# Performance work log

Hardware: AMD Instinct MI355X
Metric: run time of the kernel (lower is better)

The kernel has to match this reference:

```python
import jax, jax.numpy as jnp
import numpy as np

NUM_HEADS = 3
WIN = 7            # window_size (square)
PAD = WIN // 2     # conv / v padding


def setup_inputs() -> dict:
    key = jax.random.key(0)
    ks = jax.random.split(key, 8)
    B, C, H, W = 8, 96, 56, 56
    hd = C // NUM_HEADS  # 32
    x = jax.random.normal(ks[0], (B, C, H, W), jnp.float32)
    # qkv 1x1 conv: weight (3C, C), bias (3C,)
    w_qkv = jax.random.normal(ks[1], (3 * C, C), jnp.float32) * (C ** -0.5)
    b_qkv = jax.random.normal(ks[2], (3 * C,), jnp.float32) * 0.01
    fan_in = 2 * hd * WIN * WIN
    w_dm = jax.random.normal(ks[3], (WIN * WIN, 2 * hd, WIN, WIN), jnp.float32) * (fan_in ** -0.5)
    b_dm = jax.random.normal(ks[4], (WIN * WIN,), jnp.float32) * 0.01
    bias_table = jax.random.normal(ks[5], (WIN * WIN, NUM_HEADS), jnp.float32) * 0.02
    # proj 1x1 conv
    w_proj = jax.random.normal(ks[6], (C, C), jnp.float32) * (C ** -0.5)
    b_proj = jax.random.normal(ks[7], (C,), jnp.float32) * 0.01
    return dict(x=x, w_qkv=w_qkv, b_qkv=b_qkv, w_dm=w_dm, b_dm=b_dm,
                bias_table=bias_table, w_proj=w_proj, b_proj=b_proj)


def reference(x, w_qkv, b_qkv, w_dm, b_dm, bias_table, w_proj, b_proj):
    B, C, H, W = x.shape
    nh = NUM_HEADS
    hd = C // nh
    scale = hd ** -0.5

    # qkv 1x1 conv -> (B, 3, nh, hd, H, W)
    qkv = jnp.einsum('oc,bchw->bohw', w_qkv, x) + b_qkv[None, :, None, None]
    qkv = qkv.reshape(B, 3, nh, hd, H, W)
    q, k, v = qkv[:, 0], qkv[:, 1], qkv[:, 2]

    qk = jnp.concatenate([(q * scale).reshape(B * nh, hd, H, W),
                          k.reshape(B * nh, hd, H, W)], axis=1)
    attn = jax.lax.conv_general_dilated(
        qk, w_dm, window_strides=(1, 1), padding=[(PAD, PAD), (PAD, PAD)],
        dimension_numbers=('NCHW', 'OIHW', 'NCHW')) + b_dm[None, :, None, None]
    attn = attn.reshape(B, nh, WIN * WIN, H, W)

    # relative position bias, broadcast over spatial dims
    attn = attn + bias_table.T.reshape(1, nh, WIN * WIN, 1, 1)
    attn = jax.nn.softmax(attn, axis=2)

    # gather sliding windows of v from a zero-padded tensor
    v_pad = jnp.pad(v, ((0, 0), (0, 0), (0, 0), (PAD, PAD), (PAD, PAD)))
    vw = jnp.stack([v_pad[..., i // WIN:i // WIN + H, i % WIN:i % WIN + W]
                    for i in range(WIN * WIN)], axis=3)

    # weighted sum over window dim, merge heads back to channels
    out = jnp.sum(vw * attn[:, :, None], axis=3).reshape(B, C, H, W)

    # output 1x1 projection (dropout p=0 -> identity)
    out = jnp.einsum('oc,bchw->bohw', w_proj, out) + b_proj[None, :, None, None]
    return out
```

## Files before the change

kernel.cpp:

```cpp
#include <hip/hip_runtime.h>
#include <hip/hip_bf16.h>
#include <stdint.h>

#define BATCH 8
#define CCH 96
#define NH 3
#define HD 32
#define HGT 56
#define WID 56
#define HW 3136
#define WIN 7
#define KK 49
#define PADR 3
#define NIMG 24
#define C2 64

typedef const float* fp32p;
typedef __attribute__((ext_vector_type(8))) short bf16x8;
typedef __attribute__((ext_vector_type(16))) float f32x16;
typedef __attribute__((ext_vector_type(2))) float f32x2;
typedef unsigned short ushort_t;

__device__ __forceinline__ float bf2f_bits(unsigned u){ return __uint_as_float(u << 16); }
__device__ __forceinline__ ushort_t f2bf_bits(float f){
  __hip_bfloat16 hb = __float2bfloat16(f);
  return *(ushort_t*)&hb;
}

__global__ __launch_bounds__(256) void prep_kernel(fp32p w_dm, fp32p b_dm,
    fp32p bias_table, fp32p w_qkv, fp32p w_proj,
    __hip_bfloat16* __restrict__ w3, float* __restrict__ bias3,
    ushort_t* __restrict__ wq3, ushort_t* __restrict__ wp3){
  int t = blockIdx.x * 256 + threadIdx.x;
  if (t < 200704){
    int j   = t & 7;
    int l   = (t >> 3) & 63;
    int mt  = (t >> 9) & 1;
    int cb  = (t >> 10) & 1;
    int pt  = t >> 11;
    int pass = pt / KK, tap = pt % KK;
    int o  = mt*32 + (l & 31);
    int ch = pass*32 + cb*16 + (l >> 5)*8 + j;
    float v = 0.f;
    if (o < KK) v = w_dm[((size_t)(o*C2 + ch))*KK + tap];
    w3[t] = __float2bfloat16(v);
  } else if (t < 200896){
    int t2 = t - 200704;
    int h = t2 >> 6;
    int o = t2 & 63;
    bias3[t2] = (o < KK) ? (b_dm[o] + bias_table[o*NH + h]) : -1e30f;
  } else if (t < 200896 + 27648){
    int i = t - 200896;
    int j = i & 7, l = (i >> 3) & 63;
    int rest = i >> 9;
    int mt = rest % 9, k = rest / 9;
    int o = mt*32 + (l & 31);
    int c = k*16 + (l >> 5)*8 + j;
    wq3[i] = f2bf_bits(w_qkv[o*CCH + c]);
  } else if (t < 200896 + 27648 + 9216){
    int i = t - 200896 - 27648;
    int j = i & 7, l = (i >> 3) & 63;
    int rest = i >> 9;
    int mt = rest % 3, k = rest / 3;
    int o = mt*32 + (l & 31);
    int c = k*16 + (l >> 5)*8 + j;
    wp3[i] = f2bf_bits(w_proj[o*CCH + c]);
  }
}

__global__ __launch_bounds__(64) void qkv_kernel(fp32p x,
    const ushort_t* __restrict__ wq3, fp32p b_qkv,
    ushort_t* __restrict__ qplane, ushort_t* __restrict__ kplane,
    ushort_t* __restrict__ v2){
  __shared__ float lds[32*97];
  int wid = blockIdx.x;
  int g  = wid / 784;
  int pt = wid % 784;
  int l = threadIdx.x & 63, col = l & 31, hi = l >> 5;
  int b = pt / 98;
  int pp0 = (pt % 98) * 32;
  int pp = pp0 + col;

  #pragma unroll
  for (int it = 0; it < 48; ++it){
    int s = (int)threadIdx.x + it*64;
    int c = s >> 5, pxi = s & 31;
    lds[pxi*97 + c] = x[((size_t)b*CCH + c)*HW + pp0 + pxi];
  }
  __syncthreads();

  bf16x8 B[6];
  #pragma unroll
  for (int k = 0; k < 6; ++k){
    unsigned u[4];
    #pragma unroll
    for (int q = 0; q < 4; ++q){
      float f0 = lds[col*97 + k*16 + hi*8 + 2*q];
      float f1 = lds[col*97 + k*16 + hi*8 + 2*q + 1];
      u[q] = (unsigned)f2bf_bits(f0) | ((unsigned)f2bf_bits(f1) << 16);
    }
    unsigned* bp = (unsigned*)&B[k];
    bp[0] = u[0]; bp[1] = u[1]; bp[2] = u[2]; bp[3] = u[3];
  }

  f32x16 acc[3];
  #pragma unroll
  for (int m = 0; m < 3; ++m)
    #pragma unroll
    for (int r = 0; r < 16; ++r) acc[m][r] = 0.f;

  #pragma unroll
  for (int k = 0; k < 6; ++k){
    #pragma unroll
    for (int m = 0; m < 3; ++m){
      bf16x8 A = *(const bf16x8*)((const char*)wq3 + ((size_t)((k*9 + g*3 + m)*64 + l))*16);
      acc[m] = __builtin_amdgcn_mfma_f32_32x32x16_bf16(A, B[k], acc[m], 0, 0, 0);
    }
  }
  const float scale = 0.17677669529663687f;
  ushort_t* plane = (g == 0) ? qplane : (g == 1 ? kplane : v2);
  #pragma unroll
  for (int m = 0; m < 3; ++m){
    ushort_t* dst = plane + ((size_t)((b*NH + m)*HW + pp))*32;
    #pragma unroll
    for (int q = 0; q < 4; ++q){
      int base = 8*q + 4*hi;
      float v0 = acc[m][q*4+0] + b_qkv[g*96 + m*32 + base + 0];
      float v1 = acc[m][q*4+1] + b_qkv[g*96 + m*32 + base + 1];
      float v2f = acc[m][q*4+2] + b_qkv[g*96 + m*32 + base + 2];
      float v3 = acc[m][q*4+3] + b_qkv[g*96 + m*32 + base + 3];
      if (g == 0){ v0 *= scale; v1 *= scale; v2f *= scale; v3 *= scale; }
      uint2 pk;
      pk.x = (unsigned)f2bf_bits(v0) | ((unsigned)f2bf_bits(v1) << 16);
      pk.y = (unsigned)f2bf_bits(v2f) | ((unsigned)f2bf_bits(v3) << 16);
      *(uint2*)(&dst[base]) = pk;
    }
  }
}

#define MFMA4K(Ab, Bb) \
  { _Pragma("unroll") for (int nt = 0; nt < 2; ++nt){ \
      acc[0][nt] = __builtin_amdgcn_mfma_f32_32x32x16_bf16(Ab[0], Bb[nt], acc[0][nt], 0, 0, 0); \
      acc[1][nt] = __builtin_amdgcn_mfma_f32_32x32x16_bf16(Ab[1], Bb[nt], acc[1][nt], 0, 0, 0); \
    } }

#define LOADAK(tt, Ab) \
  { const char* An_ = Abase + (size_t)(tt)*4096; \
    Ab[0] = *(const bf16x8*)(An_); \
    Ab[1] = *(const bf16x8*)(An_ + 1024); }

#define LOADBK(tt, Bb) \
  { int ky_ = (tt) / 7, kx_ = (tt) - ky_*7; \
    _Pragma("unroll") for (int nt = 0; nt < 2; ++nt){ \
      int xp_ = nt*32 + col + kx_; if (xp_ > 61) xp_ = 61; \
      int base_ = ((row + ky_)*64 + xp_)*64; \
      int sx_ = (xp_ & 3) ^ ((xp_ >> 2) & 3); \
      Bb[nt] = *(const bf16x8*)(&smem[base_ + ((((cbw << 1) | hi) ^ sx_) << 4)]); } }

#define XWRITE(A0v, A1v) \
  { _Pragma("unroll") for (int q = 0; q < 4; ++q){ \
      float4 v4; \
      v4.x=A0v[4*q+0]; v4.y=A0v[4*q+1]; v4.z=A0v[4*q+2]; v4.w=A0v[4*q+3]; \
      *(float4*)((char*)xch + slot_o*256 + (((2*q+hi) ^ xsw)<<4)) = v4; \
      v4.x=A1v[4*q+0]; v4.y=A1v[4*q+1]; v4.z=A1v[4*q+2]; v4.w=A1v[4*q+3]; \
      *(float4*)((char*)xch + slot_o*256 + (((8+2*q+hi) ^ xsw)<<4)) = v4; } }

#define XREAD(A0v, A1v) \
  { _Pragma("unroll") for (int q = 0; q < 4; ++q){ \
      float4 v4 = *(const float4*)((char*)xch + slot_s*256 + (((2*q+hi) ^ xsw)<<4)); \
      A0v[4*q+0]+=v4.x; A0v[4*q+1]+=v4.y; A0v[4*q+2]+=v4.z; A0v[4*q+3]+=v4.w; \
      v4 = *(const float4*)((char*)xch + slot_s*256 + (((8+2*q+hi) ^ xsw)<<4)); \
      A1v[4*q+0]+=v4.x; A1v[4*q+1]+=v4.y; A1v[4*q+2]+=v4.z; A1v[4*q+3]+=v4.w; } }

__global__ __launch_bounds__(256, 3) void attn_kernel(
    const ushort_t* __restrict__ qplane, const ushort_t* __restrict__ kplane,
    const __hip_bfloat16* __restrict__ w3, const float* __restrict__ bias3,
    const ushort_t* __restrict__ v2, ushort_t* __restrict__ tmp2){
  __shared__ char smem[50176];

  int d = blockIdx.x;
  int bid = (d & 7)*84 + (d >> 3);
  int n  = bid / 28;
  int y0 = (bid % 28) * 2;
  int b = n / NH, head = n % NH;
  int tid = threadIdx.x;
  int l = tid & 63, w = tid >> 6, hi = l >> 5, col = l & 31;
  int row = w >> 1;
  int cbw = w & 1;

  f32x16 acc[2][2];
  #pragma unroll
  for (int r = 0; r < 16; ++r){
    int rowv = (r & 3) + 8*(r >> 2) + 4*hi;
    float b0 = (cbw == 0) ? bias3[head*64 + rowv] : 0.f;
    float b1 = (cbw == 0) ? bias3[head*64 + 32 + rowv] : 0.f;
    #pragma unroll
    for (int nt = 0; nt < 2; ++nt){ acc[0][nt][r] = b0; acc[1][nt][r] = b1; }
  }

  for (int pass = 0; pass < 2; ++pass){
    if (pass) __syncthreads();
    const char* src = (const char*)(pass ? kplane : qplane) + (size_t)n * HW * 64;
    #pragma unroll
    for (int it = 0; it < 8; ++it){
      int s = tid + it*256;
      int c   = s & 3;
      int xp  = (s >> 2) & 63;
      int rw  = s >> 8;
      int gy = y0 - 3 + rw;
      int gx = xp - 3;
      uint4 val = {0,0,0,0};
      if ((unsigned)gy < HGT && (unsigned)gx < WID)
        val = *(const uint4*)(src + (size_t)(gy*WID + gx)*64 + c*16);
      int sw = (c ^ (xp & 3) ^ ((xp >> 2) & 3)) << 4;
      *(uint4*)(&smem[(rw*64 + xp)*64 + sw]) = val;
    }
    __syncthreads();

    const char* Abase = (const char*)w3 + (size_t)pass*KK*4096 + cbw*2048 + l*16;
    bf16x8 A0[2], A1[2], B0[2], B1[2];
    LOADAK(0, A0); LOADBK(0, B0);
    LOADAK(1, A1); LOADBK(1, B1);
    for (int t = 0; t < 48; t += 2){
      MFMA4K(A0, B0);
      LOADAK(t+2, A0); LOADBK(t+2, B0);
      MFMA4K(A1, B1);
      int t3 = (t+3 < KK) ? (t+3) : 48;
      LOADAK(t3, A1); LOADBK(t3, B1);
    }
    MFMA4K(A0, B0);
  }

  __syncthreads();
  float* xch = (float*)smem;
  int xsw = col & 15;
  {
    int slot_o = row*64 + (1-cbw)*32 + col;
    if (cbw == 0){ XWRITE(acc[0][1], acc[1][1]); }
    else         { XWRITE(acc[0][0], acc[1][0]); }
  }
  __syncthreads();
  f32x16 a0, a1;
  {
    int slot_s = row*64 + cbw*32 + col;
    if (cbw == 0){ XREAD(acc[0][0], acc[1][0]); a0 = acc[0][0]; a1 = acc[1][0]; }
    else         { XREAD(acc[0][1], acc[1][1]); a0 = acc[0][1]; a1 = acc[1][1]; }
  }

  const char* vb = (const char*)v2 + (size_t)n * HW * 64;
  uint4 vreg[8];
  #pragma unroll
  for (int it = 0; it < 8; ++it){
    int s = tid + it*256;
    int xp  = s & 63;
    int c   = (s >> 6) & 3;
    int rw  = s >> 8;
    int gy = y0 - 3 + rw;
    int gx = xp - 3;
    uint4 val = {0,0,0,0};
    if ((unsigned)gy < HGT && (unsigned)gx < WID)
      val = *(const uint4*)(vb + (size_t)(gy*WID + gx)*64 + c*16);
    vreg[it] = val;
  }

  ushort_t* Pp = (ushort_t*)&smem[32768];
  {
    float m = -1e30f;
    #pragma unroll
    for (int r = 0; r < 16; ++r){ m = fmaxf(m, a0[r]); m = fmaxf(m, a1[r]); }
    m = fmaxf(m, __shfl_xor(m, 32));
    float s = 0.f;
    #pragma unroll
    for (int r = 0; r < 16; ++r){
      a0[r] = __expf(a0[r] - m); s += a0[r];
      a1[r] = __expf(a1[r] - m); s += a1[r];
    }
    s += __shfl_xor(s, 32);
    float inv = 1.f / s;
    int pixslot = row*64 + cbw*32 + col;
    ushort_t* Pr = Pp + pixslot*68;
    #pragma unroll
    for (int q = 0; q < 4; ++q){
      int base = 8*q + 4*hi;
      uint2 pk0;
      pk0.x = (unsigned)f2bf_bits(a0[q*4+0]*inv) | ((unsigned)f2bf_bits(a0[q*4+1]*inv) << 16);
      pk0.y = (unsigned)f2bf_bits(a0[q*4+2]*inv) | ((unsigned)f2bf_bits(a0[q*4+3]*inv) << 16);
      *(uint2*)(&Pr[base]) = pk0;
      uint2 pk1;
      pk1.x = (unsigned)f2bf_bits(a1[q*4+0]*inv) | ((unsigned)f2bf_bits(a1[q*4+1]*inv) << 16);
      pk1.y = (unsigned)f2bf_bits(a1[q*4+2]*inv) | ((unsigned)f2bf_bits(a1[q*4+3]*inv) << 16);
      *(uint2*)(&Pr[32 + base]) = pk1;
    }
  }
  __syncthreads();

  #pragma unroll
  for (int it = 0; it < 8; ++it){
    int s = tid + it*256;
    int xp  = s & 63;
    int c   = (s >> 6) & 3;
    int rw  = s >> 8;
    *(uint4*)(&smem[((c*8 + rw)*64 + xp)*16]) = vreg[it];
  }
  __syncthreads();

  int ch2 = tid >> 7;
  int slot = tid & 127;
  int pr = slot >> 6, pxx = slot & 63;
  if (pxx < WID){
    f32x2 out2[8];
    #pragma unroll
    for (int i = 0; i < 8; ++i){ out2[i].x = 0.f; out2[i].y = 0.f; }
    #pragma unroll
    for (int ky = 0; ky < WIN; ++ky){
      #pragma unroll
      for (int kx = 0; kx < WIN; ++kx){
        float pw = bf2f_bits(Pp[slot*68 + ky*7 + kx]);
        f32x2 pw2; pw2.x = pw; pw2.y = pw;
        int vrow = pr + ky, xp = pxx + kx;
        #pragma unroll
        for (int ci = 0; ci < 2; ++ci){
          int cc = ch2*2 + ci;
          uint4 vv = *(const uint4*)(&smem[((cc*8 + vrow)*64 + xp)*16]);
          unsigned ua[4] = {vv.x, vv.y, vv.z, vv.w};
          #pragma unroll
          for (int q = 0; q < 4; ++q){
            f32x2 v2f;
            v2f.x = __uint_as_float(ua[q] << 16);
            v2f.y = __uint_as_float(ua[q] & 0xffff0000u);
            out2[ci*4 + q] += pw2 * v2f;
          }
        }
      }
    }
    int pp = (y0 + pr)*WID + pxx;
    ushort_t* dst = tmp2 + ((size_t)(b*HW + pp))*96 + head*32 + ch2*16;
    #pragma unroll
    for (int j2 = 0; j2 < 2; ++j2){
      unsigned u[4];
      #pragma unroll
      for (int q = 0; q < 4; ++q){
        u[q] = (unsigned)f2bf_bits(out2[j2*4 + q].x) | ((unsigned)f2bf_bits(out2[j2*4 + q].y) << 16);
      }
      uint4 w4; w4.x=u[0]; w4.y=u[1]; w4.z=u[2]; w4.w=u[3];
      *(uint4*)(&dst[j2*8]) = w4;
    }
  }
}

__global__ __launch_bounds__(64) void proj_kernel(const ushort_t* __restrict__ tmp2,
    const ushort_t* __restrict__ wp3, fp32p b_proj, float* __restrict__ outp){
  int pt = blockIdx.x;
  int l = threadIdx.x & 63, col = l & 31, hi = l >> 5;
  int px = pt*32 + col;
  int b = px / HW, pp = px % HW;

  bf16x8 B[6];
  const char* bb = (const char*)tmp2 + (size_t)px*192 + hi*16;
  #pragma unroll
  for (int k = 0; k < 6; ++k) B[k] = *(const bf16x8*)(bb + k*32);

  f32x16 acc[3];
  #pragma unroll
  for (int m = 0; m < 3; ++m)
    #pragma unroll
    for (int r = 0; r < 16; ++r) acc[m][r] = 0.f;

  #pragma unroll
  for (int k = 0; k < 6; ++k){
    #pragma unroll
    for (int m = 0; m < 3; ++m){
      bf16x8 A = *(const bf16x8*)((const char*)wp3 + ((size_t)((k*3 + m)*64 + l))*16);
      acc[m] = __builtin_amdgcn_mfma_f32_32x32x16_bf16(A, B[k], acc[m], 0, 0, 0);
    }
  }
  #pragma unroll
  for (int m = 0; m < 3; ++m){
    #pragma unroll
    for (int r = 0; r < 16; ++r){
      int o = m*32 + (r & 3) + 8*(r >> 2) + 4*hi;
      outp[((size_t)(b*CCH + o))*HW + pp] = acc[m][r] + b_proj[o];
    }
  }
}

extern "C" void kernel_launch(void* const* d_in, const int* in_sizes, int n_in,
                              void* d_out, int out_size, void* d_ws, size_t ws_size,
                              hipStream_t stream){
  fp32p x          = (fp32p)d_in[0];
  fp32p w_qkv      = (fp32p)d_in[1];
  fp32p b_qkv      = (fp32p)d_in[2];
  fp32p w_dm       = (fp32p)d_in[3];
  fp32p b_dm       = (fp32p)d_in[4];
  fp32p bias_table = (fp32p)d_in[5];
  fp32p w_proj     = (fp32p)d_in[6];
  fp32p b_proj     = (fp32p)d_in[7];

  char* ws = (char*)d_ws;
  const size_t PLANE_BYTES = (size_t)NIMG * HW * 32 * 2;
  const size_t TMP2_BYTES  = (size_t)BATCH * HW * 96 * 2;
  const size_t W3_BYTES    = 200704ull * 2;
  size_t off = 0;
  ushort_t* qplane = (ushort_t*)(ws + off); off += PLANE_BYTES;
  ushort_t* kplane = (ushort_t*)(ws + off); off += PLANE_BYTES;
  ushort_t* v2     = (ushort_t*)(ws + off); off += PLANE_BYTES;
  ushort_t* tmp2   = (ushort_t*)(ws + off); off += TMP2_BYTES;
  __hip_bfloat16* w3 = (__hip_bfloat16*)(ws + off); off += W3_BYTES;
  float* bias3     = (float*)(ws + off);    off += 192*4;
  ushort_t* wq3    = (ushort_t*)(ws + off); off += 27648*2;
  ushort_t* wp3    = (ushort_t*)(ws + off); off += 9216*2;

  hipLaunchKernelGGL(prep_kernel, dim3(929), dim3(256), 0, stream,
                     w_dm, b_dm, bias_table, w_qkv, w_proj, w3, bias3, wq3, wp3);
  hipLaunchKernelGGL(qkv_kernel, dim3(2352), dim3(64), 0, stream,
                     x, wq3, b_qkv, qplane, kplane, v2);
  hipLaunchKernelGGL(attn_kernel, dim3(672), dim3(256), 0, stream,
                     qplane, kplane, w3, bias3, v2, tmp2);
  hipLaunchKernelGGL(proj_kernel, dim3(784), dim3(64), 0, stream,
                     tmp2, wp3, b_proj, (float*)d_out);
}
```

Before: 71.25 us.

## Fuse weight prep into qkv kernel and share x tile across q/k/v

Merges the weight-preparation kernel and the qkv projection kernel into one launch: the first 784 blocks compute qkv with three wavefronts (one per q/k/v group) sharing a single LDS tile of x, and the remaining blocks repack w_dm, bias and w_proj. The qkv weights are now read directly from fp32 and converted to bf16 in registers, so the separate wq3 staging buffer is dropped. The aims are to remove one kernel launch and to avoid loading each x tile three times. In exchange, every qkv block redoes the weight conversion and issues uncoalesced fp32 weight loads.

```diff
diff --git a/kernel.cpp b/kernel.cpp
--- a/kernel.cpp
+++ b/kernel.cpp
@@ -27,63 +27,56 @@
   return *(ushort_t*)&hb;
 }
 
-__global__ __launch_bounds__(256) void prep_kernel(fp32p w_dm, fp32p b_dm,
-    fp32p bias_table, fp32p w_qkv, fp32p w_proj,
+__global__ __launch_bounds__(192) void qkv_prep_kernel(fp32p x, fp32p w_qkv,
+    fp32p b_qkv, fp32p w_dm, fp32p b_dm, fp32p bias_table, fp32p w_proj,
+    ushort_t* __restrict__ qplane, ushort_t* __restrict__ kplane,
+    ushort_t* __restrict__ v2,
     __hip_bfloat16* __restrict__ w3, float* __restrict__ bias3,
-    ushort_t* __restrict__ wq3, ushort_t* __restrict__ wp3){
-  int t = blockIdx.x * 256 + threadIdx.x;
-  if (t < 200704){
-    int j   = t & 7;
-    int l   = (t >> 3) & 63;
-    int mt  = (t >> 9) & 1;
-    int cb  = (t >> 10) & 1;
-    int pt  = t >> 11;
-    int pass = pt / KK, tap = pt % KK;
-    int o  = mt*32 + (l & 31);
-    int ch = pass*32 + cb*16 + (l >> 5)*8 + j;
-    float v = 0.f;
-    if (o < KK) v = w_dm[((size_t)(o*C2 + ch))*KK + tap];
-    w3[t] = __float2bfloat16(v);
-  } else if (t < 200896){
-    int t2 = t - 200704;
-    int h = t2 >> 6;
-    int o = t2 & 63;
-    bias3[t2] = (o < KK) ? (b_dm[o] + bias_table[o*NH + h]) : -1e30f;
-  } else if (t < 200896 + 27648){
-    int i = t - 200896;
-    int j = i & 7, l = (i >> 3) & 63;
-    int rest = i >> 9;
-    int mt = rest % 9, k = rest / 9;
-    int o = mt*32 + (l & 31);
-    int c = k*16 + (l >> 5)*8 + j;
-    wq3[i] = f2bf_bits(w_qkv[o*CCH + c]);
-  } else if (t < 200896 + 27648 + 9216){
-    int i = t - 200896 - 27648;
-    int j = i & 7, l = (i >> 3) & 63;
-    int rest = i >> 9;
-    int mt = rest % 3, k = rest / 3;
-    int o = mt*32 + (l & 31);
-    int c = k*16 + (l >> 5)*8 + j;
-    wp3[i] = f2bf_bits(w_proj[o*CCH + c]);
-  }
-}
-
-__global__ __launch_bounds__(64) void qkv_kernel(fp32p x,
-    const ushort_t* __restrict__ wq3, fp32p b_qkv,
-    ushort_t* __restrict__ qplane, ushort_t* __restrict__ kplane,
-    ushort_t* __restrict__ v2){
+    ushort_t* __restrict__ wp3){
   __shared__ float lds[32*97];
-  int wid = blockIdx.x;
-  int g  = wid / 784;
-  int pt = wid % 784;
-  int l = threadIdx.x & 63, col = l & 31, hi = l >> 5;
+  int bx = blockIdx.x;
+  if (bx >= 784){
+    int t = (bx - 784)*192 + (int)threadIdx.x;
+    if (t < 200704){
+      int j   = t & 7;
+      int l   = (t >> 3) & 63;
+      int mt  = (t >> 9) & 1;
+      int cb  = (t >> 10) & 1;
+      int pt  = t >> 11;
+      int pass = pt / KK, tap = pt % KK;
+      int o  = mt*32 + (l & 31);
+      int ch = pass*32 + cb*16 + (l >> 5)*8 + j;
+      float v = 0.f;
+      if (o < KK) v = w_dm[((size_t)(o*C2 + ch))*KK + tap];
+      w3[t] = __float2bfloat16(v);
+    } else if (t < 200896){
+      int t2 = t - 200704;
+      int h = t2 >> 6;
+      int o = t2 & 63;
+      bias3[t2] = (o < KK) ? (b_dm[o] + bias_table[o*NH + h]) : -1e30f;
+    } else if (t < 210112){
+      int i = t - 200896;
+      int j = i & 7, l = (i >> 3) & 63;
+      int rest = i >> 9;
+      int mt = rest % 3, k = rest / 3;
+      int o = mt*32 + (l & 31);
+      int c = k*16 + (l >> 5)*8 + j;
+      wp3[i] = f2bf_bits(w_proj[o*CCH + c]);
+    }
+    return;
+  }
+
+  int pt = bx;
+  int tid = threadIdx.x;
+  int g  = tid >> 6;
+  int l = tid & 63, col = l & 31, hi = l >> 5;
   int b = pt / 98;
   int pp0 = (pt % 98) * 32;
   int pp = pp0 + col;
 
   #pragma unroll
-  for (int it = 0; it < 48; ++it){
-    int s = (int)threadIdx.x + it*64;
+  for (int it = 0; it < 16; ++it){
+    int s = tid + it*192;
     int c = s >> 5, pxi = s & 31;
     lds[pxi*97 + c] = x[((size_t)b*CCH + c)*HW + pp0 + pxi];
   }
@@ -113,7 +106,17 @@
   for (int k = 0; k < 6; ++k){
     #pragma unroll
     for (int m = 0; m < 3; ++m){
-      bf16x8 A = *(const bf16x8*)((const char*)wq3 + ((size_t)((k*9 + g*3 + m)*64 + l))*16);
+      const float* wr = w_qkv + (size_t)((g*3 + m)*32 + col)*CCH + k*16 + hi*8;
+      float4 f0 = *(const float4*)wr;
+      float4 f1 = *(const float4*)(wr + 4);
+      unsigned ua[4];
+      ua[0] = (unsigned)f2bf_bits(f0.x) | ((unsigned)f2bf_bits(f0.y) << 16);
+      ua[1] = (unsigned)f2bf_bits(f0.z) | ((unsigned)f2bf_bits(f0.w) << 16);
+      ua[2] = (unsigned)f2bf_bits(f1.x) | ((unsigned)f2bf_bits(f1.y) << 16);
+      ua[3] = (unsigned)f2bf_bits(f1.z) | ((unsigned)f2bf_bits(f1.w) << 16);
+      bf16x8 A;
+      unsigned* ap = (unsigned*)&A;
+      ap[0] = ua[0]; ap[1] = ua[1]; ap[2] = ua[2]; ap[3] = ua[3];
       acc[m] = __builtin_amdgcn_mfma_f32_32x32x16_bf16(A, B[k], acc[m], 0, 0, 0);
     }
   }
@@ -407,13 +410,11 @@
   ushort_t* tmp2   = (ushort_t*)(ws + off); off += TMP2_BYTES;
   __hip_bfloat16* w3 = (__hip_bfloat16*)(ws + off); off += W3_BYTES;
   float* bias3     = (float*)(ws + off);    off += 192*4;
-  ushort_t* wq3    = (ushort_t*)(ws + off); off += 27648*2;
   ushort_t* wp3    = (ushort_t*)(ws + off); off += 9216*2;
 
-  hipLaunchKernelGGL(prep_kernel, dim3(929), dim3(256), 0, stream,
-                     w_dm, b_dm, bias_table, w_qkv, w_proj, w3, bias3, wq3, wp3);
-  hipLaunchKernelGGL(qkv_kernel, dim3(2352), dim3(64), 0, stream,
-                     x, wq3, b_qkv, qplane, kplane, v2);
+  hipLaunchKernelGGL(qkv_prep_kernel, dim3(1879), dim3(192), 0, stream,
+                     x, w_qkv, b_qkv, w_dm, b_dm, bias_table, w_proj,
+                     qplane, kplane, v2, w3, bias3, wp3);
   hipLaunchKernelGGL(attn_kernel, dim3(672), dim3(256), 0, stream,
                      qplane, kplane, w3, bias3, v2, tmp2);
   hipLaunchKernelGGL(proj_kernel, dim3(784), dim3(64), 0, stream,
```

Measured after the change: 79.06 us. 1.11x slower.
